# Kernel tuning notes

Hardware: AMD Instinct MI355X
Metric: run time of the kernel (lower is better)

Reference implementation:

```python
import jax, jax.numpy as jnp
import numpy as np

VOCAB, EMB, H, TRK, L, BOUND = 50257, 1024, 1024, 1024, 256, 25

def setup_inputs() -> dict:
    key = jax.random.key(0)
    ks = jax.random.split(key, 16)
    s = 0.02
    return {
        "query_words": jax.random.normal(ks[0], (L, 1, H), jnp.float32),
        "query_vector": jax.random.normal(ks[1], (1, 1, TRK), jnp.float32),
        "decision_vector": jax.random.normal(ks[2], (1, 1, H), jnp.float32),
        "target_answer": jax.random.randint(ks[3], (BOUND, 1, 1), 0, VOCAB, jnp.int64),
        "emb_table": jax.random.normal(ks[4], (VOCAB, EMB), jnp.float32) * s,
        "gru_Wih": jax.random.normal(ks[5], (3 * H, EMB + TRK), jnp.float32) * s,
        "gru_Whh": jax.random.normal(ks[6], (3 * H, H), jnp.float32) * s,
        "gru_bih": jnp.zeros((3 * H,), jnp.float32),
        "gru_bhh": jnp.zeros((3 * H,), jnp.float32),
        "attn_Wq": jax.random.normal(ks[7], (H, H), jnp.float32) * s,
        "attn_bq": jnp.zeros((H,), jnp.float32),
        "attn_Wk": jax.random.normal(ks[8], (H, H), jnp.float32) * s,
        "attn_bk": jnp.zeros((H,), jnp.float32),
        "attn_v": jax.random.normal(ks[9], (H,), jnp.float32) * s,
        "concat_W": jax.random.normal(ks[10], (H, 2 * H), jnp.float32) * s,
        "concat_b": jnp.zeros((H,), jnp.float32),
        "out_W": jax.random.normal(ks[11], (VOCAB, H), jnp.float32) * s,
        "out_b": jnp.zeros((VOCAB,), jnp.float32),
    }


def reference(query_words, query_vector, decision_vector, target_answer,
              emb_table, gru_Wih, gru_Whh, gru_bih, gru_bhh,
              attn_Wq, attn_bq, attn_Wk, attn_bk, attn_v,
              concat_W, concat_b, out_W, out_b):
    # eval-mode: dropout = identity; tf_ratio=1 -> teacher forcing for all steps
    h_dim = decision_vector.shape[-1]
    qw = query_words[:, 0, :]                      # [L, H] encoder memory
    keys = qw @ attn_Wk.T + attn_bk                # precompute key projection once
    qv = query_vector.reshape(-1)                  # [TRK]
    h0 = decision_vector.reshape(-1)               # [H]
    ta = target_answer.reshape(-1).astype(jnp.int32)
    # input token per step: SOS (0), then teacher-forced targets
    idx_seq = jnp.concatenate([jnp.zeros((1,), jnp.int32), ta[: BOUND - 1]])

    def step(h, idx):
        x = jnp.concatenate([qv, emb_table[idx]])  # cat(query_vector, embedded)
        g = gru_Wih @ x + gru_bih                  # [3H]
        gh = gru_Whh @ h + gru_bhh                 # [3H]
        r = jax.nn.sigmoid(g[:h_dim] + gh[:h_dim])
        z = jax.nn.sigmoid(g[h_dim:2 * h_dim] + gh[h_dim:2 * h_dim])
        n = jnp.tanh(g[2 * h_dim:] + r * gh[2 * h_dim:])
        h_new = (1.0 - z) * n + z * h
        # additive (Bahdanau) attention over query_words
        e = jnp.tanh(keys + attn_Wq @ h_new + attn_bq) @ attn_v  # [L]
        w = jax.nn.softmax(e)
        ctx = w @ qw                                              # [H]
        vec = jnp.tanh(concat_W @ jnp.concatenate([h_new, ctx]) + concat_b)
        logits = out_W @ vec + out_b                              # [VOCAB]
        return h_new, jax.nn.log_softmax(logits)

    _, logps = jax.lax.scan(step, h0, idx_seq)     # [BOUND, VOCAB]
    answer = jnp.argmax(logps, axis=-1)            # greedy tokens per step
    return (answer, logps)
```

## Files before the change

kernel.cpp:

```cpp
#include <hip/hip_runtime.h>
#include <math.h>

#define VOCAB 50257
#define EMB 1024
#define HD 1024
#define TRK 1024
#define LQ 256
#define BND 25

__device__ __forceinline__ float wred(float s){
  #pragma unroll
  for (int m = 32; m >= 1; m >>= 1) s += __shfl_xor(s, m, 64);
  return s;
}

__global__ __launch_bounds__(256) void k_pre(const float* __restrict__ Wih,
                                             const float* __restrict__ qv,
                                             const float* __restrict__ bih,
                                             const int*   __restrict__ ta,
                                             const float* __restrict__ emb,
                                             float* __restrict__ gib,
                                             float* __restrict__ E){
  int b = blockIdx.x, tid = threadIdx.x;
  if (b < 768){
    int w = tid >> 6, lane = tid & 63;
    int row = b*4 + w;
    const float* a = Wih + (size_t)row*2048;
    float s = 0.f;
    #pragma unroll
    for (int e = 0; e < 4; e++){
      int k = e*256 + lane*4;
      float4 av = *(const float4*)(a + k);
      float4 qr = *(const float4*)(qv + k);
      s += av.x*qr.x + av.y*qr.y + av.z*qr.z + av.w*qr.w;
    }
    s = wred(s);
    if (lane == 0) gib[row] = s + bih[row];
  } else {
    int g = (b - 768)*256 + tid;
    int t = g >> 10, i = g & 1023;
    int idx = (t == 0) ? 0 : ta[t-1];
    E[g] = emb[(size_t)idx*EMB + i];
  }
}

__global__ __launch_bounds__(256) void k_keys(const float* __restrict__ qw,
                                              const float* __restrict__ Wk,
                                              float* __restrict__ part){
  __shared__ float qt[64*256];
  int jb = blockIdx.x;
  int ks = blockIdx.y;
  int tid = threadIdx.x;
  int l = tid;
  float acc[16];
  #pragma unroll
  for (int j = 0; j < 16; j++) acc[j] = 0.f;

  for (int kt = 0; kt < 4; kt++){
    int kb = ks*256 + kt*64;
    __syncthreads();
    #pragma unroll
    for (int p = 0; p < 16; p++){
      int fidx = (p*256 + tid)*4;
      int kk = fidx & 63, ll = fidx >> 6;
      float4 v = *(const float4*)(qw + (size_t)ll*1024 + kb + kk);
      qt[(kk+0)*256 + (ll ^ ((kk+0)&31))] = v.x;
      qt[(kk+1)*256 + (ll ^ ((kk+1)&31))] = v.y;
      qt[(kk+2)*256 + (ll ^ ((kk+2)&31))] = v.z;
      qt[(kk+3)*256 + (ll ^ ((kk+3)&31))] = v.w;
    }
    __syncthreads();
    #pragma unroll
    for (int s = 0; s < 4; s++){
      float qr[16];
      #pragma unroll
      for (int q = 0; q < 16; q++){
        int k = s*16 + q;
        qr[q] = qt[k*256 + (l ^ (k&31))];
      }
      #pragma unroll
      for (int j = 0; j < 16; j++){
        const float* wr = Wk + (size_t)(jb*16 + j)*1024 + kb + s*16;
        #pragma unroll
        for (int q4 = 0; q4 < 4; q4++){
          float4 wv = *(const float4*)(wr + q4*4);
          acc[j] += qr[q4*4+0]*wv.x + qr[q4*4+1]*wv.y
                  + qr[q4*4+2]*wv.z + qr[q4*4+3]*wv.w;
        }
      }
    }
  }
  #pragma unroll
  for (int j = 0; j < 16; j++)
    part[((size_t)ks*1024 + jb*16 + j)*256 + l] = acc[j];
}

__global__ __launch_bounds__(256) void k_keys_red(const float* __restrict__ part,
                                                  const float* __restrict__ bk,
                                                  float* __restrict__ keysT){
  int g = blockIdx.x*256 + threadIdx.x;
  int base = g*4;
  float4 s0 = *(const float4*)(part + base);
  float4 s1 = *(const float4*)(part + 262144 + base);
  float4 s2 = *(const float4*)(part + 524288 + base);
  float4 s3 = *(const float4*)(part + 786432 + base);
  float b = bk[base >> 8];
  float4 r;
  r.x = s0.x + s1.x + s2.x + s3.x + b;
  r.y = s0.y + s1.y + s2.y + s3.y + b;
  r.z = s0.z + s1.z + s2.z + s3.z + b;
  r.w = s0.w + s1.w + s2.w + s3.w + b;
  *(float4*)(keysT + base) = r;
}

template<int K, int NCH>
__global__ __launch_bounds__(256) void k_gemm_s2(const float* __restrict__ A, int lda,
                                                 const float* __restrict__ B, int ldb,
                                                 const float* __restrict__ bias,
                                                 float* __restrict__ C,
                                                 int R, int N, int act){
  __shared__ float Bl[NCH*K];
  constexpr int KD4 = K/4;
  int tid = threadIdx.x, w = tid >> 6, lane = tid & 63;
  int row = blockIdx.x*4 + w;
  const float* a = A + (size_t)row*lda;
  float4 ar[K/256];
  #pragma unroll
  for (int e = 0; e < K/256; e++)
    ar[e] = *(const float4*)(a + e*256 + lane*4);
  float bs = bias[row];
  for (int c0 = 0; c0 < N; c0 += NCH){
    int nt = min(NCH, N - c0);
    __syncthreads();
    int total = nt*KD4;
    for (int i = tid; i < total; i += 256){
      int j = i/KD4, kk = i - j*KD4;
      *(float4*)&Bl[j*K + kk*4] = *(const float4*)(B + (size_t)(c0+j)*ldb + kk*4);
    }
    __syncthreads();
    for (int j = 0; j < nt; j++){
      float s = 0.f;
      #pragma unroll
      for (int e = 0; e < K/256; e++){
        float4 bv = *(const float4*)&Bl[j*K + e*256 + lane*4];
        s += ar[e].x*bv.x + ar[e].y*bv.y + ar[e].z*bv.z + ar[e].w*bv.w;
      }
      s = wred(s);
      if (lane == 0){
        float v = s + bs;
        if (act) v = tanhf(v);
        C[(size_t)(c0+j)*R + row] = v;
      }
    }
  }
}

__global__ __launch_bounds__(256, 2) void k_gru4(const float* __restrict__ Whh,
                                                 const float* __restrict__ bhh,
                                                 const float* __restrict__ gi,
                                                 const float* __restrict__ dv,
                                                 float* __restrict__ HC,
                                                 float* __restrict__ hx){
  __shared__ float Wl[12][1024];
  __shared__ float hbuf[1024];
  __shared__ float sres[12];
  int tid = threadIdx.x, w = tid >> 6, lane = tid & 63;
  int b = blockIdx.x;
  for (int i = tid; i < 3072; i += 256){
    int r = i >> 8, c = (i & 255)*4;
    int g = r >> 2, s = r & 3;
    *(float4*)&Wl[r][c] = *(const float4*)(Whh + (size_t)(g*1024 + b*4 + s)*1024 + c);
  }
  *(float4*)&hbuf[tid*4] = *(const float4*)(dv + tid*4);
  __syncthreads();

  for (int t = 0; t < BND; t++){
    float g0=0,g1=0,g2=0,bb0=0,bb1=0,bb2=0,hpown=0;
    if (tid < 4){
      int i = b*4 + tid;
      const float* gg = gi + (size_t)t*3072;
      g0 = gg[i]; g1 = gg[1024+i]; g2 = gg[2048+i];
      bb0 = bhh[i]; bb1 = bhh[1024+i]; bb2 = bhh[2048+i];
      hpown = hbuf[i];
    }
    float hv[16];
    #pragma unroll
    for (int e = 0; e < 4; e++){
      float4 v = *(const float4*)&hbuf[e*256 + lane*4];
      hv[e*4]=v.x; hv[e*4+1]=v.y; hv[e*4+2]=v.z; hv[e*4+3]=v.w;
    }
    #pragma unroll
    for (int j = 0; j < 3; j++){
      int r = w*3 + j;
      float a = 0.f;
      #pragma unroll
      for (int e = 0; e < 4; e++){
        float4 v = *(const float4*)&Wl[r][e*256 + lane*4];
        a += v.x*hv[e*4] + v.y*hv[e*4+1] + v.z*hv[e*4+2] + v.w*hv[e*4+3];
      }
      a = wred(a);
      if (lane == 0) sres[r] = a;
    }
    __syncthreads();
    if (tid < 4){
      int i = b*4 + tid;
      float ghr = sres[tid]   + bb0;
      float ghz = sres[4+tid] + bb1;
      float ghn = sres[8+tid] + bb2;
      float rr = 1.f/(1.f + expf(-(g0 + ghr)));
      float zz = 1.f/(1.f + expf(-(g1 + ghz)));
      float nn = tanhf(g2 + rr*ghn);
      float hnew = (1.f - zz)*nn + zz*hpown;
      HC[(size_t)t*2048 + i] = hnew;
      if (t < BND-1){
        __hip_atomic_store(hx + b*8 + tid, hnew, __ATOMIC_RELAXED, __HIP_MEMORY_SCOPE_AGENT);
        asm volatile("s_waitcnt vmcnt(0)" ::: "memory");
      }
    }
    if (t == BND-1) break;
    __syncthreads();
    if (tid == 0)
      __hip_atomic_store((int*)(hx + b*8 + 4), t+1, __ATOMIC_RELAXED, __HIP_MEMORY_SCOPE_AGENT);
    if (w == 0){
      for (;;){
        int f0 = __hip_atomic_load((const int*)(hx + (lane      )*8 + 4), __ATOMIC_RELAXED, __HIP_MEMORY_SCOPE_AGENT);
        int f1 = __hip_atomic_load((const int*)(hx + (64  + lane)*8 + 4), __ATOMIC_RELAXED, __HIP_MEMORY_SCOPE_AGENT);
        int f2 = __hip_atomic_load((const int*)(hx + (128 + lane)*8 + 4), __ATOMIC_RELAXED, __HIP_MEMORY_SCOPE_AGENT);
        int f3 = __hip_atomic_load((const int*)(hx + (192 + lane)*8 + 4), __ATOMIC_RELAXED, __HIP_MEMORY_SCOPE_AGENT);
        if (min(min(f0,f1),min(f2,f3)) >= t+1) break;
        __builtin_amdgcn_s_sleep(1);
      }
      #pragma unroll
      for (int q = 0; q < 4; q++){
        float d0 = __hip_atomic_load(hx + (q*64 + lane)*8 + 0, __ATOMIC_RELAXED, __HIP_MEMORY_SCOPE_AGENT);
        float d1 = __hip_atomic_load(hx + (q*64 + lane)*8 + 1, __ATOMIC_RELAXED, __HIP_MEMORY_SCOPE_AGENT);
        float d2 = __hip_atomic_load(hx + (q*64 + lane)*8 + 2, __ATOMIC_RELAXED, __HIP_MEMORY_SCOPE_AGENT);
        float d3 = __hip_atomic_load(hx + (q*64 + lane)*8 + 3, __ATOMIC_RELAXED, __HIP_MEMORY_SCOPE_AGENT);
        hbuf[q*256 + lane*4 + 0] = d0;
        hbuf[q*256 + lane*4 + 1] = d1;
        hbuf[q*256 + lane*4 + 2] = d2;
        hbuf[q*256 + lane*4 + 3] = d3;
      }
    }
    __syncthreads();
  }
}

__global__ __launch_bounds__(256) void k_attn1(const float* __restrict__ keysT,
                                               const float* __restrict__ Qt,
                                               const float* __restrict__ av,
                                               float* __restrict__ epart){
  int t = blockIdx.x, jc = blockIdx.y;
  int l = threadIdx.x;
  const float* q = Qt + (size_t)t*1024;
  int j0 = jc*32;
  float acc = 0.f;
  #pragma unroll
  for (int u = 0; u < 8; u++){
    int j = j0 + u*4;
    float k0 = keysT[(size_t)(j+0)*256 + l];
    float k1 = keysT[(size_t)(j+1)*256 + l];
    float k2 = keysT[(size_t)(j+2)*256 + l];
    float k3 = keysT[(size_t)(j+3)*256 + l];
    acc += tanhf(k0 + q[j+0]) * av[j+0]
         + tanhf(k1 + q[j+1]) * av[j+1]
         + tanhf(k2 + q[j+2]) * av[j+2]
         + tanhf(k3 + q[j+3]) * av[j+3];
  }
  epart[((size_t)t*32 + jc)*256 + l] = acc;
}

__global__ __launch_bounds__(256) void k_attn2(const float* __restrict__ epart,
                                               const float* __restrict__ qw,
                                               float* __restrict__ HC){
  __shared__ float red[256];
  __shared__ float sw[256];
  int t = blockIdx.x, tid = threadIdx.x;
  float e = 0.f;
  for (int jc = 0; jc < 32; jc++) e += epart[((size_t)t*32 + jc)*256 + tid];
  red[tid] = e; __syncthreads();
  for (int s = 128; s > 0; s >>= 1){
    if (tid < s) red[tid] = fmaxf(red[tid], red[tid+s]);
    __syncthreads();
  }
  float m = red[0]; __syncthreads();
  float wv = expf(e - m);
  red[tid] = wv; __syncthreads();
  for (int s = 128; s > 0; s >>= 1){
    if (tid < s) red[tid] += red[tid+s];
    __syncthreads();
  }
  float inv = 1.f/red[0];
  sw[tid] = wv*inv; __syncthreads();
  float4 c = make_float4(0.f,0.f,0.f,0.f);
  const float* qp = qw + tid*4;
  for (int ll = 0; ll < 256; ll++){
    float wl = sw[ll];
    float4 v = *(const float4*)(qp + (size_t)ll*1024);
    c.x += wl*v.x; c.y += wl*v.y; c.z += wl*v.z; c.w += wl*v.w;
  }
  *(float4*)(HC + (size_t)t*2048 + 1024 + tid*4) = c;
}

__global__ __launch_bounds__(256, 1) void k_gemm_big9(const float* __restrict__ A,
                                                      const float* __restrict__ B,
                                                      const float* __restrict__ bias,
                                                      float* __restrict__ C){
  __shared__ float Bl[25600];
  int tid = threadIdx.x;
  int rl = tid & 63;
  int q  = tid >> 6;
  int R0 = blockIdx.x*256;

  for (int i = tid; i < 6400; i += 256){
    int t = i >> 8, kk = (i & 255) << 2;
    *(float4*)&Bl[t*1024 + kk] = *(const float4*)(B + (size_t)t*1024 + kk);
  }

  const float* ap[4];
  #pragma unroll
  for (int j = 0; j < 4; j++){
    int r = R0 + 64*j + rl;
    if (r >= VOCAB) r = VOCAB-1;
    ap[j] = A + (size_t)r*1024 + q*256;
  }

  float acc[4][25];
  #pragma unroll
  for (int j = 0; j < 4; j++)
    #pragma unroll
    for (int t = 0; t < 25; t++) acc[j][t] = 0.f;

  float4 a[4][4];
  #pragma unroll
  for (int j = 0; j < 4; j++){
    a[j][0] = *(const float4*)(ap[j] + 0);
    a[j][1] = *(const float4*)(ap[j] + 4);
    a[j][2] = *(const float4*)(ap[j] + 8);
    a[j][3] = *(const float4*)(ap[j] + 12);
  }
  __syncthreads();

  const float* bq = Bl + q*256;
  #pragma unroll 1
  for (int kb = 0; kb < 256; kb += 16){
    float4 n[4][4];
    if (kb + 16 < 256){
      #pragma unroll
      for (int j = 0; j < 4; j++){
        n[j][0] = *(const float4*)(ap[j] + kb + 16);
        n[j][1] = *(const float4*)(ap[j] + kb + 20);
        n[j][2] = *(const float4*)(ap[j] + kb + 24);
        n[j][3] = *(const float4*)(ap[j] + kb + 28);
      }
    }
    #pragma unroll
    for (int t = 0; t < 25; t++){
      const float* bt = bq + t*1024 + kb;
      float4 b0 = *(const float4*)(bt + 0);
      float4 b1 = *(const float4*)(bt + 4);
      float4 b2 = *(const float4*)(bt + 8);
      float4 b3 = *(const float4*)(bt + 12);
      #pragma unroll
      for (int j = 0; j < 4; j++){
        acc[j][t] += a[j][0].x*b0.x + a[j][0].y*b0.y + a[j][0].z*b0.z + a[j][0].w*b0.w
                   + a[j][1].x*b1.x + a[j][1].y*b1.y + a[j][1].z*b1.z + a[j][1].w*b1.w
                   + a[j][2].x*b2.x + a[j][2].y*b2.y + a[j][2].z*b2.z + a[j][2].w*b2.w
                   + a[j][3].x*b3.x + a[j][3].y*b3.y + a[j][3].z*b3.z + a[j][3].w*b3.w;
      }
    }
    #pragma unroll
    for (int j = 0; j < 4; j++){
      a[j][0] = n[j][0]; a[j][1] = n[j][1]; a[j][2] = n[j][2]; a[j][3] = n[j][3];
    }
  }

  for (int tc0 = 0; tc0 < 25; tc0 += 13){
    int nt = min(13, 25 - tc0);
    __syncthreads();
    #pragma unroll
    for (int j = 0; j < 4; j++)
      for (int tt = 0; tt < nt; tt++)
        Bl[(q*256 + j*64 + rl)*13 + tt] = acc[j][tc0 + tt];
    __syncthreads();
    for (int v = tid; v < 256*nt; v += 256){
      int rr = v & 255, tt = v >> 8;
      float s = 0.f;
      #pragma unroll
      for (int qq = 0; qq < 4; qq++)
        s += Bl[(qq*256 + rr)*13 + tt];
      int row = R0 + rr;
      if (row < VOCAB)
        C[(size_t)(tc0 + tt)*VOCAB + row] = s + bias[row];
    }
  }
}

__global__ __launch_bounds__(256) void k_lstat(const float* __restrict__ C,
                                               float* __restrict__ pm,
                                               float* __restrict__ ps,
                                               int*   __restrict__ pa){
  __shared__ float sm[256], ss[256];
  __shared__ int   sa[256];
  int t = blockIdx.x, c = blockIdx.y, tid = threadIdx.x;
  int r0 = c*6283, r1 = min(r0 + 6283, VOCAB);
  const float* p = C + (size_t)t*VOCAB;
  float m = -3.4e38f, s = 0.f; int arg = r0;
  for (int r = r0 + tid; r < r1; r += 256){
    float x = p[r];
    if (x > m){ s = s*expf(m - x) + 1.f; m = x; arg = r; }
    else       s += expf(x - m);
  }
  sm[tid] = m; ss[tid] = s; sa[tid] = arg; __syncthreads();
  for (int st = 128; st > 0; st >>= 1){
    if (tid < st){
      float m1 = sm[tid], s1 = ss[tid]; int a1 = sa[tid];
      float m2 = sm[tid+st], s2 = ss[tid+st]; int a2 = sa[tid+st];
      if (m2 > m1){ sm[tid] = m2; ss[tid] = s2 + s1*expf(m1 - m2); sa[tid] = a2; }
      else if (m2 == m1){ ss[tid] = s1 + s2; sa[tid] = min(a1, a2); }
      else { ss[tid] = s1 + s2*expf(m2 - m1); }
    }
    __syncthreads();
  }
  if (tid == 0){ pm[t*8 + c] = sm[0]; ps[t*8 + c] = ss[0]; pa[t*8 + c] = sa[0]; }
}

__global__ void k_lfin(const float* __restrict__ pm, const float* __restrict__ ps,
                       const int* __restrict__ pa, float* __restrict__ Lg,
                       float* __restrict__ out){
  int t = threadIdx.x;
  if (t < 25){
    float M = pm[t*8], S = ps[t*8]; int A = pa[t*8];
    for (int c = 1; c < 8; c++){
      float m2 = pm[t*8+c], s2 = ps[t*8+c]; int a2 = pa[t*8+c];
      if (m2 > M){ S = s2 + S*expf(M - m2); M = m2; A = a2; }
      else if (m2 == M){ S += s2; A = min(A, a2); }
      else S += s2*expf(m2 - M);
    }
    Lg[t] = logf(S) + M;
    out[t] = (float)A;
  }
}

__global__ __launch_bounds__(256) void k_lsub(float* __restrict__ C,
                                              const float* __restrict__ Lg){
  int t = blockIdx.y;
  int r = blockIdx.x*256 + threadIdx.x;
  if (r < VOCAB) C[(size_t)t*VOCAB + r] -= Lg[t];
}

extern "C" void kernel_launch(void* const* d_in, const int* in_sizes, int n_in,
                              void* d_out, int out_size, void* d_ws, size_t ws_size,
                              hipStream_t stream){
  const float* qw  = (const float*)d_in[0];
  const float* qv  = (const float*)d_in[1];
  const float* dv  = (const float*)d_in[2];
  const int*   ta  = (const int*)d_in[3];
  const float* emb = (const float*)d_in[4];
  const float* Wih = (const float*)d_in[5];
  const float* Whh = (const float*)d_in[6];
  const float* bih = (const float*)d_in[7];
  const float* bhh = (const float*)d_in[8];
  const float* Wq  = (const float*)d_in[9];
  const float* bq  = (const float*)d_in[10];
  const float* Wk  = (const float*)d_in[11];
  const float* bk  = (const float*)d_in[12];
  const float* av  = (const float*)d_in[13];
  const float* cW  = (const float*)d_in[14];
  const float* cb  = (const float*)d_in[15];
  const float* oW  = (const float*)d_in[16];
  const float* ob  = (const float*)d_in[17];
  float* out = (float*)d_out;
  float* ws  = (float*)d_ws;

  float* part  = ws;
  float* ep    = ws;
  float* pm    = ws;
  float* ps    = ws + 256;
  int*   pa    = (int*)(ws + 512);
  float* Lg    = ws + 768;
  float* keysT = ws + 1048576;
  float* E     = ws + 1310720;
  float* gib   = ws + 1336320;
  float* gi    = ws + 1339392;
  float* HC    = ws + 1416192;
  float* Qt    = ws + 1467392;
  float* VEC   = ws + 1492992;
  float* hx    = ws + 1518592;

  hipMemsetAsync(hx, 0, 2048*4, stream);
  k_pre<<<868, 256, 0, stream>>>(Wih, qv, bih, ta, emb, gib, E);
  k_keys<<<dim3(64,4), 256, 0, stream>>>(qw, Wk, part);
  k_keys_red<<<256, 256, 0, stream>>>(part, bk, keysT);
  k_gemm_s2<1024,16><<<768, 256, 0, stream>>>(Wih + 1024, 2048, E, 1024, gib, gi, 3072, 25, 0);
  k_gru4<<<256, 256, 0, stream>>>(Whh, bhh, gi, dv, HC, hx);
  k_gemm_s2<1024,16><<<256, 256, 0, stream>>>(Wq, 1024, HC, 2048, bq, Qt, 1024, 25, 0);
  k_attn1<<<dim3(25,32), 256, 0, stream>>>(keysT, Qt, av, ep);
  k_attn2<<<25, 256, 0, stream>>>(ep, qw, HC);
  k_gemm_s2<2048,8><<<256, 256, 0, stream>>>(cW, 2048, HC, 2048, cb, VEC, 1024, 25, 1);
  k_gemm_big9<<<197, 256, 0, stream>>>(oW, VEC, ob, out + 25);
  k_lstat<<<dim3(25,8), 256, 0, stream>>>(out + 25, pm, ps, pa);
  k_lfin<<<1, 64, 0, stream>>>(pm, ps, pa, Lg, out);
  k_lsub<<<dim3(197,25), 256, 0, stream>>>(out + 25, Lg);
}
```

Measured before the change: 424.1 us.

## Split output-projection GEMM along K into two halves for more blocks

The vocab projection GEMM is split along the reduction dimension: each row tile gets two blocks, each covering half of K, with smaller shared memory. The two partial results are written to a workspace buffer and to the output, then summed with the bias inside the log-softmax stat and subtract kernels. This doubles the block count from 197 to 394 so more of the GPU's compute units are busy. The cost is extra traffic for the second partial logits array, read in both the stat and subtract passes.

```diff
diff --git a/kernel.cpp b/kernel.cpp
--- a/kernel.cpp
+++ b/kernel.cpp
@@ -302,19 +302,21 @@
   *(float4*)(HC + (size_t)t*2048 + 1024 + tid*4) = c;
 }
 
-__global__ __launch_bounds__(256, 1) void k_gemm_big9(const float* __restrict__ A,
-                                                      const float* __restrict__ B,
-                                                      const float* __restrict__ bias,
-                                                      float* __restrict__ C){
-  __shared__ float Bl[25600];
+__global__ __launch_bounds__(256, 1) void k_gemm_big10(const float* __restrict__ A,
+                                                       const float* __restrict__ B,
+                                                       float* __restrict__ P0,
+                                                       float* __restrict__ P1){
+  __shared__ float Bl[13312];
   int tid = threadIdx.x;
   int rl = tid & 63;
   int q  = tid >> 6;
-  int R0 = blockIdx.x*256;
-
-  for (int i = tid; i < 6400; i += 256){
-    int t = i >> 8, kk = (i & 255) << 2;
-    *(float4*)&Bl[t*1024 + kk] = *(const float4*)(B + (size_t)t*1024 + kk);
+  int half = blockIdx.x & 1;
+  int R0 = (blockIdx.x >> 1)*256;
+  float* P = half ? P1 : P0;
+
+  for (int i = tid; i < 3200; i += 256){
+    int t = i >> 7, kk = (i & 127) << 2;
+    *(float4*)&Bl[t*512 + kk] = *(const float4*)(B + (size_t)t*1024 + half*512 + kk);
   }
 
   const float* ap[4];
@@ -322,7 +324,7 @@
   for (int j = 0; j < 4; j++){
     int r = R0 + 64*j + rl;
     if (r >= VOCAB) r = VOCAB-1;
-    ap[j] = A + (size_t)r*1024 + q*256;
+    ap[j] = A + (size_t)r*1024 + half*512 + q*128;
   }
 
   float acc[4][25];
@@ -341,11 +343,11 @@
   }
   __syncthreads();
 
-  const float* bq = Bl + q*256;
+  const float* bq = Bl + q*128;
   #pragma unroll 1
-  for (int kb = 0; kb < 256; kb += 16){
+  for (int kb = 0; kb < 128; kb += 16){
     float4 n[4][4];
-    if (kb + 16 < 256){
+    if (kb + 16 < 128){
       #pragma unroll
       for (int j = 0; j < 4; j++){
         n[j][0] = *(const float4*)(ap[j] + kb + 16);
@@ -356,7 +358,7 @@
     }
     #pragma unroll
     for (int t = 0; t < 25; t++){
-      const float* bt = bq + t*1024 + kb;
+      const float* bt = bq + t*512 + kb;
       float4 b0 = *(const float4*)(bt + 0);
       float4 b1 = *(const float4*)(bt + 4);
       float4 b2 = *(const float4*)(bt + 8);
@@ -391,12 +393,14 @@
         s += Bl[(qq*256 + rr)*13 + tt];
       int row = R0 + rr;
       if (row < VOCAB)
-        C[(size_t)(tc0 + tt)*VOCAB + row] = s + bias[row];
-    }
-  }
-}
-
-__global__ __launch_bounds__(256) void k_lstat(const float* __restrict__ C,
+        P[(size_t)(tc0 + tt)*VOCAB + row] = s;
+    }
+  }
+}
+
+__global__ __launch_bounds__(256) void k_lstat(const float* __restrict__ P0,
+                                               const float* __restrict__ P1,
+                                               const float* __restrict__ ob,
                                                float* __restrict__ pm,
                                                float* __restrict__ ps,
                                                int*   __restrict__ pa){
@@ -404,10 +408,11 @@
   __shared__ int   sa[256];
   int t = blockIdx.x, c = blockIdx.y, tid = threadIdx.x;
   int r0 = c*6283, r1 = min(r0 + 6283, VOCAB);
-  const float* p = C + (size_t)t*VOCAB;
+  const float* p0 = P0 + (size_t)t*VOCAB;
+  const float* p1 = P1 + (size_t)t*VOCAB;
   float m = -3.4e38f, s = 0.f; int arg = r0;
   for (int r = r0 + tid; r < r1; r += 256){
-    float x = p[r];
+    float x = p0[r] + p1[r] + ob[r];
     if (x > m){ s = s*expf(m - x) + 1.f; m = x; arg = r; }
     else       s += expf(x - m);
   }
@@ -442,11 +447,16 @@
   }
 }
 
-__global__ __launch_bounds__(256) void k_lsub(float* __restrict__ C,
+__global__ __launch_bounds__(256) void k_lsub(const float* __restrict__ P0,
+                                              float* __restrict__ C,
+                                              const float* __restrict__ ob,
                                               const float* __restrict__ Lg){
   int t = blockIdx.y;
   int r = blockIdx.x*256 + threadIdx.x;
-  if (r < VOCAB) C[(size_t)t*VOCAB + r] -= Lg[t];
+  if (r < VOCAB){
+    size_t idx = (size_t)t*VOCAB + r;
+    C[idx] = P0[idx] + C[idx] + ob[r] - Lg[t];
+  }
 }
 
 extern "C" void kernel_launch(void* const* d_in, const int* in_sizes, int n_in,
@@ -475,10 +485,7 @@
 
   float* part  = ws;
   float* ep    = ws;
-  float* pm    = ws;
-  float* ps    = ws + 256;
-  int*   pa    = (int*)(ws + 512);
-  float* Lg    = ws + 768;
+  float* P0    = ws;
   float* keysT = ws + 1048576;
   float* E     = ws + 1310720;
   float* gib   = ws + 1336320;
@@ -487,6 +494,10 @@
   float* Qt    = ws + 1467392;
   float* VEC   = ws + 1492992;
   float* hx    = ws + 1518592;
+  float* pm    = ws + 1520640;
+  float* ps    = ws + 1520896;
+  int*   pa    = (int*)(ws + 1521152);
+  float* Lg    = ws + 1521408;
 
   hipMemsetAsync(hx, 0, 2048*4, stream);
   k_pre<<<868, 256, 0, stream>>>(Wih, qv, bih, ta, emb, gib, E);
@@ -498,8 +509,8 @@
   k_attn1<<<dim3(25,32), 256, 0, stream>>>(keysT, Qt, av, ep);
   k_attn2<<<25, 256, 0, stream>>>(ep, qw, HC);
   k_gemm_s2<2048,8><<<256, 256, 0, stream>>>(cW, 2048, HC, 2048, cb, VEC, 1024, 25, 1);
-  k_gemm_big9<<<197, 256, 0, stream>>>(oW, VEC, ob, out + 25);
-  k_lstat<<<dim3(25,8), 256, 0, stream>>>(out + 25, pm, ps, pa);
+  k_gemm_big10<<<394, 256, 0, stream>>>(oW, VEC, P0, out + 25);
+  k_lstat<<<dim3(25,8), 256, 0, stream>>>(P0, out + 25, ob, pm, ps, pa);
   k_lfin<<<1, 64, 0, stream>>>(pm, ps, pa, Lg, out);
-  k_lsub<<<dim3(197,25), 256, 0, stream>>>(out + 25, Lg);
-}
+  k_lsub<<<dim3(197,25), 256, 0, stream>>>(P0, out + 25, ob, Lg);
+}
```

After: 445.5 us. 1.05x slower.

## Use sentinel-valued per-step hidden buffers for GRU sync; split output GEMM K across 8 waves

Applied to the files above, without the earlier changes.

The GRU recurrence no longer uses per-block step flags with a barrier and a flag-polling loop. Each step writes hidden values into a fresh per-timestep slot pre-filled with a sentinel pattern, and readers spin until the data words themselves are not the sentinel, which removes a barrier and a round of flag traffic per step. The large vocabulary GEMM now runs 512-thread blocks, with each wave covering 128 K elements instead of 256, doubling in-block parallelism and shortening each thread's K loop. In exchange the final reduction across waves is larger, the memset now clears a much bigger buffer, and a float whose bit pattern equals the sentinel is nudged by one bit.

```diff
diff --git a/kernel.cpp b/kernel.cpp
--- a/kernel.cpp
+++ b/kernel.cpp
@@ -7,6 +7,7 @@
 #define TRK 1024
 #define LQ 256
 #define BND 25
+#define SENT 0xAAAAAAAAu
 
 __device__ __forceinline__ float wred(float s){
   #pragma unroll
@@ -155,12 +156,12 @@
   }
 }
 
-__global__ __launch_bounds__(256, 2) void k_gru4(const float* __restrict__ Whh,
+__global__ __launch_bounds__(256, 2) void k_gru5(const float* __restrict__ Whh,
                                                  const float* __restrict__ bhh,
                                                  const float* __restrict__ gi,
                                                  const float* __restrict__ dv,
                                                  float* __restrict__ HC,
-                                                 float* __restrict__ hx){
+                                                 unsigned* __restrict__ hxu){
   __shared__ float Wl[12][1024];
   __shared__ float hbuf[1024];
   __shared__ float sres[12];
@@ -213,33 +214,31 @@
       float hnew = (1.f - zz)*nn + zz*hpown;
       HC[(size_t)t*2048 + i] = hnew;
       if (t < BND-1){
-        __hip_atomic_store(hx + b*8 + tid, hnew, __ATOMIC_RELAXED, __HIP_MEMORY_SCOPE_AGENT);
+        union { float f; unsigned u; } cv; cv.f = hnew;
+        if (cv.u == SENT) cv.u ^= 1u;
+        __hip_atomic_store(hxu + (size_t)t*2048 + b*8 + tid, cv.u,
+                           __ATOMIC_RELAXED, __HIP_MEMORY_SCOPE_AGENT);
         asm volatile("s_waitcnt vmcnt(0)" ::: "memory");
       }
     }
     if (t == BND-1) break;
-    __syncthreads();
-    if (tid == 0)
-      __hip_atomic_store((int*)(hx + b*8 + 4), t+1, __ATOMIC_RELAXED, __HIP_MEMORY_SCOPE_AGENT);
     if (w == 0){
-      for (;;){
-        int f0 = __hip_atomic_load((const int*)(hx + (lane      )*8 + 4), __ATOMIC_RELAXED, __HIP_MEMORY_SCOPE_AGENT);
-        int f1 = __hip_atomic_load((const int*)(hx + (64  + lane)*8 + 4), __ATOMIC_RELAXED, __HIP_MEMORY_SCOPE_AGENT);
-        int f2 = __hip_atomic_load((const int*)(hx + (128 + lane)*8 + 4), __ATOMIC_RELAXED, __HIP_MEMORY_SCOPE_AGENT);
-        int f3 = __hip_atomic_load((const int*)(hx + (192 + lane)*8 + 4), __ATOMIC_RELAXED, __HIP_MEMORY_SCOPE_AGENT);
-        if (min(min(f0,f1),min(f2,f3)) >= t+1) break;
-        __builtin_amdgcn_s_sleep(1);
-      }
+      const unsigned* base = hxu + (size_t)t*2048;
       #pragma unroll
       for (int q = 0; q < 4; q++){
-        float d0 = __hip_atomic_load(hx + (q*64 + lane)*8 + 0, __ATOMIC_RELAXED, __HIP_MEMORY_SCOPE_AGENT);
-        float d1 = __hip_atomic_load(hx + (q*64 + lane)*8 + 1, __ATOMIC_RELAXED, __HIP_MEMORY_SCOPE_AGENT);
-        float d2 = __hip_atomic_load(hx + (q*64 + lane)*8 + 2, __ATOMIC_RELAXED, __HIP_MEMORY_SCOPE_AGENT);
-        float d3 = __hip_atomic_load(hx + (q*64 + lane)*8 + 3, __ATOMIC_RELAXED, __HIP_MEMORY_SCOPE_AGENT);
-        hbuf[q*256 + lane*4 + 0] = d0;
-        hbuf[q*256 + lane*4 + 1] = d1;
-        hbuf[q*256 + lane*4 + 2] = d2;
-        hbuf[q*256 + lane*4 + 3] = d3;
+        int line = q*64 + lane;
+        unsigned d0, d1, d2, d3;
+        for (;;){
+          d0 = __hip_atomic_load(base + line*8 + 0, __ATOMIC_RELAXED, __HIP_MEMORY_SCOPE_AGENT);
+          d1 = __hip_atomic_load(base + line*8 + 1, __ATOMIC_RELAXED, __HIP_MEMORY_SCOPE_AGENT);
+          d2 = __hip_atomic_load(base + line*8 + 2, __ATOMIC_RELAXED, __HIP_MEMORY_SCOPE_AGENT);
+          d3 = __hip_atomic_load(base + line*8 + 3, __ATOMIC_RELAXED, __HIP_MEMORY_SCOPE_AGENT);
+          if (d0 != SENT && d1 != SENT && d2 != SENT && d3 != SENT) break;
+        }
+        hbuf[line*4 + 0] = __uint_as_float(d0);
+        hbuf[line*4 + 1] = __uint_as_float(d1);
+        hbuf[line*4 + 2] = __uint_as_float(d2);
+        hbuf[line*4 + 3] = __uint_as_float(d3);
       }
     }
     __syncthreads();
@@ -302,17 +301,17 @@
   *(float4*)(HC + (size_t)t*2048 + 1024 + tid*4) = c;
 }
 
-__global__ __launch_bounds__(256, 1) void k_gemm_big9(const float* __restrict__ A,
-                                                      const float* __restrict__ B,
-                                                      const float* __restrict__ bias,
-                                                      float* __restrict__ C){
-  __shared__ float Bl[25600];
+__global__ __launch_bounds__(512, 1) void k_gemm_big12(const float* __restrict__ A,
+                                                       const float* __restrict__ B,
+                                                       const float* __restrict__ bias,
+                                                       float* __restrict__ C){
+  __shared__ float Bl[26624];
   int tid = threadIdx.x;
   int rl = tid & 63;
-  int q  = tid >> 6;
+  int w  = tid >> 6;
   int R0 = blockIdx.x*256;
 
-  for (int i = tid; i < 6400; i += 256){
+  for (int i = tid; i < 6400; i += 512){
     int t = i >> 8, kk = (i & 255) << 2;
     *(float4*)&Bl[t*1024 + kk] = *(const float4*)(B + (size_t)t*1024 + kk);
   }
@@ -322,7 +321,7 @@
   for (int j = 0; j < 4; j++){
     int r = R0 + 64*j + rl;
     if (r >= VOCAB) r = VOCAB-1;
-    ap[j] = A + (size_t)r*1024 + q*256;
+    ap[j] = A + (size_t)r*1024 + w*128;
   }
 
   float acc[4][25];
@@ -341,11 +340,11 @@
   }
   __syncthreads();
 
-  const float* bq = Bl + q*256;
+  const float* bw = Bl + w*128;
   #pragma unroll 1
-  for (int kb = 0; kb < 256; kb += 16){
+  for (int kb = 0; kb < 128; kb += 16){
     float4 n[4][4];
-    if (kb + 16 < 256){
+    if (kb + 16 < 128){
       #pragma unroll
       for (int j = 0; j < 4; j++){
         n[j][0] = *(const float4*)(ap[j] + kb + 16);
@@ -356,7 +355,7 @@
     }
     #pragma unroll
     for (int t = 0; t < 25; t++){
-      const float* bt = bq + t*1024 + kb;
+      const float* bt = bw + t*1024 + kb;
       float4 b0 = *(const float4*)(bt + 0);
       float4 b1 = *(const float4*)(bt + 4);
       float4 b2 = *(const float4*)(bt + 8);
@@ -381,14 +380,14 @@
     #pragma unroll
     for (int j = 0; j < 4; j++)
       for (int tt = 0; tt < nt; tt++)
-        Bl[(q*256 + j*64 + rl)*13 + tt] = acc[j][tc0 + tt];
-    __syncthreads();
-    for (int v = tid; v < 256*nt; v += 256){
+        Bl[(w*256 + j*64 + rl)*13 + tt] = acc[j][tc0 + tt];
+    __syncthreads();
+    for (int v = tid; v < 256*nt; v += 512){
       int rr = v & 255, tt = v >> 8;
       float s = 0.f;
       #pragma unroll
-      for (int qq = 0; qq < 4; qq++)
-        s += Bl[(qq*256 + rr)*13 + tt];
+      for (int ww = 0; ww < 8; ww++)
+        s += Bl[(ww*256 + rr)*13 + tt];
       int row = R0 + rr;
       if (row < VOCAB)
         C[(size_t)(tc0 + tt)*VOCAB + row] = s + bias[row];
@@ -475,10 +474,6 @@
 
   float* part  = ws;
   float* ep    = ws;
-  float* pm    = ws;
-  float* ps    = ws + 256;
-  int*   pa    = (int*)(ws + 512);
-  float* Lg    = ws + 768;
   float* keysT = ws + 1048576;
   float* E     = ws + 1310720;
   float* gib   = ws + 1336320;
@@ -486,19 +481,23 @@
   float* HC    = ws + 1416192;
   float* Qt    = ws + 1467392;
   float* VEC   = ws + 1492992;
-  float* hx    = ws + 1518592;
-
-  hipMemsetAsync(hx, 0, 2048*4, stream);
+  unsigned* hx = (unsigned*)(ws + 1518592);
+  float* pm    = ws + 1569792;
+  float* ps    = ws + 1570048;
+  int*   pa    = (int*)(ws + 1570304);
+  float* Lg    = ws + 1570560;
+
+  hipMemsetAsync(hx, 0xAA, 51200*4, stream);
   k_pre<<<868, 256, 0, stream>>>(Wih, qv, bih, ta, emb, gib, E);
   k_keys<<<dim3(64,4), 256, 0, stream>>>(qw, Wk, part);
   k_keys_red<<<256, 256, 0, stream>>>(part, bk, keysT);
   k_gemm_s2<1024,16><<<768, 256, 0, stream>>>(Wih + 1024, 2048, E, 1024, gib, gi, 3072, 25, 0);
-  k_gru4<<<256, 256, 0, stream>>>(Whh, bhh, gi, dv, HC, hx);
+  k_gru5<<<256, 256, 0, stream>>>(Whh, bhh, gi, dv, HC, hx);
   k_gemm_s2<1024,16><<<256, 256, 0, stream>>>(Wq, 1024, HC, 2048, bq, Qt, 1024, 25, 0);
   k_attn1<<<dim3(25,32), 256, 0, stream>>>(keysT, Qt, av, ep);
   k_attn2<<<25, 256, 0, stream>>>(ep, qw, HC);
   k_gemm_s2<2048,8><<<256, 256, 0, stream>>>(cW, 2048, HC, 2048, cb, VEC, 1024, 25, 1);
-  k_gemm_big9<<<197, 256, 0, stream>>>(oW, VEC, ob, out + 25);
+  k_gemm_big12<<<197, 512, 0, stream>>>(oW, VEC, ob, out + 25);
   k_lstat<<<dim3(25,8), 256, 0, stream>>>(out + 25, pm, ps, pa);
   k_lfin<<<1, 64, 0, stream>>>(pm, ps, pa, Lg, out);
   k_lsub<<<dim3(197,25), 256, 0, stream>>>(out + 25, Lg);
```

Measured after the change: 424.4 us. No clear change (+0.1%).

## Fuse prelude kernels, use sentinel-based GRU sync with 128 larger blocks

Applied to the files above, without the earlier changes.

Merges the Wih·qv, embedding gather and key-projection kernels into one launch. The keys reduction is folded into the attention score kernel, and the log-sum finalize is folded into the subtraction kernel. The persistent GRU kernel now runs 128 blocks of 512 threads with 8 rows each. It replaces the per-step flag-then-data handshake with per-step buffers that are pre-filled with a sentinel pattern, and consumers spin until the data itself is non-sentinel. This removes launches and one round of cross-block latency per recurrent step. The costs are a larger memset, redundant partial-sum reads in attention, and reliance on the sentinel never being a real value, which is guarded by flipping a bit.

```diff
diff --git a/kernel.cpp b/kernel.cpp
--- a/kernel.cpp
+++ b/kernel.cpp
@@ -7,6 +7,7 @@
 #define TRK 1024
 #define LQ 256
 #define BND 25
+#define SENT 0xAAAAAAAAu
 
 __device__ __forceinline__ float wred(float s){
   #pragma unroll
@@ -14,13 +15,17 @@
   return s;
 }
 
-__global__ __launch_bounds__(256) void k_pre(const float* __restrict__ Wih,
-                                             const float* __restrict__ qv,
-                                             const float* __restrict__ bih,
-                                             const int*   __restrict__ ta,
-                                             const float* __restrict__ emb,
-                                             float* __restrict__ gib,
-                                             float* __restrict__ E){
+__global__ __launch_bounds__(256) void k_pre_keys(const float* __restrict__ Wih,
+                                                  const float* __restrict__ qv,
+                                                  const float* __restrict__ bih,
+                                                  const int*   __restrict__ ta,
+                                                  const float* __restrict__ emb,
+                                                  const float* __restrict__ qw,
+                                                  const float* __restrict__ Wk,
+                                                  float* __restrict__ gib,
+                                                  float* __restrict__ E,
+                                                  float* __restrict__ part){
+  __shared__ float qt[64*256];
   int b = blockIdx.x, tid = threadIdx.x;
   if (b < 768){
     int w = tid >> 6, lane = tid & 63;
@@ -36,21 +41,18 @@
     }
     s = wred(s);
     if (lane == 0) gib[row] = s + bih[row];
-  } else {
+    return;
+  }
+  if (b < 868){
     int g = (b - 768)*256 + tid;
     int t = g >> 10, i = g & 1023;
     int idx = (t == 0) ? 0 : ta[t-1];
     E[g] = emb[(size_t)idx*EMB + i];
-  }
-}
-
-__global__ __launch_bounds__(256) void k_keys(const float* __restrict__ qw,
-                                              const float* __restrict__ Wk,
-                                              float* __restrict__ part){
-  __shared__ float qt[64*256];
-  int jb = blockIdx.x;
-  int ks = blockIdx.y;
-  int tid = threadIdx.x;
+    return;
+  }
+  int b2 = b - 868;
+  int jb = b2 & 63;
+  int ks = b2 >> 6;
   int l = tid;
   float acc[16];
   #pragma unroll
@@ -93,24 +95,6 @@
   #pragma unroll
   for (int j = 0; j < 16; j++)
     part[((size_t)ks*1024 + jb*16 + j)*256 + l] = acc[j];
-}
-
-__global__ __launch_bounds__(256) void k_keys_red(const float* __restrict__ part,
-                                                  const float* __restrict__ bk,
-                                                  float* __restrict__ keysT){
-  int g = blockIdx.x*256 + threadIdx.x;
-  int base = g*4;
-  float4 s0 = *(const float4*)(part + base);
-  float4 s1 = *(const float4*)(part + 262144 + base);
-  float4 s2 = *(const float4*)(part + 524288 + base);
-  float4 s3 = *(const float4*)(part + 786432 + base);
-  float b = bk[base >> 8];
-  float4 r;
-  r.x = s0.x + s1.x + s2.x + s3.x + b;
-  r.y = s0.y + s1.y + s2.y + s3.y + b;
-  r.z = s0.z + s1.z + s2.z + s3.z + b;
-  r.w = s0.w + s1.w + s2.w + s3.w + b;
-  *(float4*)(keysT + base) = r;
 }
 
 template<int K, int NCH>
@@ -155,29 +139,30 @@
   }
 }
 
-__global__ __launch_bounds__(256, 2) void k_gru4(const float* __restrict__ Whh,
+__global__ __launch_bounds__(512, 1) void k_gru6(const float* __restrict__ Whh,
                                                  const float* __restrict__ bhh,
                                                  const float* __restrict__ gi,
                                                  const float* __restrict__ dv,
                                                  float* __restrict__ HC,
-                                                 float* __restrict__ hx){
-  __shared__ float Wl[12][1024];
+                                                 unsigned* __restrict__ hxu){
+  __shared__ float Wl[24][1024];
   __shared__ float hbuf[1024];
-  __shared__ float sres[12];
+  __shared__ float sres[24];
   int tid = threadIdx.x, w = tid >> 6, lane = tid & 63;
   int b = blockIdx.x;
-  for (int i = tid; i < 3072; i += 256){
+  for (int i = tid; i < 6144; i += 512){
     int r = i >> 8, c = (i & 255)*4;
-    int g = r >> 2, s = r & 3;
-    *(float4*)&Wl[r][c] = *(const float4*)(Whh + (size_t)(g*1024 + b*4 + s)*1024 + c);
-  }
-  *(float4*)&hbuf[tid*4] = *(const float4*)(dv + tid*4);
+    int g = r >> 3, s = r & 7;
+    *(float4*)&Wl[r][c] = *(const float4*)(Whh + (size_t)(g*1024 + b*8 + s)*1024 + c);
+  }
+  if (tid < 256)
+    *(float4*)&hbuf[tid*4] = *(const float4*)(dv + tid*4);
   __syncthreads();
 
   for (int t = 0; t < BND; t++){
     float g0=0,g1=0,g2=0,bb0=0,bb1=0,bb2=0,hpown=0;
-    if (tid < 4){
-      int i = b*4 + tid;
+    if (tid < 8){
+      int i = b*8 + tid;
       const float* gg = gi + (size_t)t*3072;
       g0 = gg[i]; g1 = gg[1024+i]; g2 = gg[2048+i];
       bb0 = bhh[i]; bb1 = bhh[1024+i]; bb2 = bhh[2048+i];
@@ -202,51 +187,52 @@
       if (lane == 0) sres[r] = a;
     }
     __syncthreads();
-    if (tid < 4){
-      int i = b*4 + tid;
-      float ghr = sres[tid]   + bb0;
-      float ghz = sres[4+tid] + bb1;
-      float ghn = sres[8+tid] + bb2;
+    if (tid < 8){
+      int i = b*8 + tid;
+      float ghr = sres[tid]      + bb0;
+      float ghz = sres[8  + tid] + bb1;
+      float ghn = sres[16 + tid] + bb2;
       float rr = 1.f/(1.f + expf(-(g0 + ghr)));
       float zz = 1.f/(1.f + expf(-(g1 + ghz)));
       float nn = tanhf(g2 + rr*ghn);
       float hnew = (1.f - zz)*nn + zz*hpown;
       HC[(size_t)t*2048 + i] = hnew;
       if (t < BND-1){
-        __hip_atomic_store(hx + b*8 + tid, hnew, __ATOMIC_RELAXED, __HIP_MEMORY_SCOPE_AGENT);
+        union { float f; unsigned u; } cv; cv.f = hnew;
+        if (cv.u == SENT) cv.u ^= 1u;
+        __hip_atomic_store(hxu + (size_t)t*2048 + b*16 + tid, cv.u,
+                           __ATOMIC_RELAXED, __HIP_MEMORY_SCOPE_AGENT);
         asm volatile("s_waitcnt vmcnt(0)" ::: "memory");
       }
     }
     if (t == BND-1) break;
-    __syncthreads();
-    if (tid == 0)
-      __hip_atomic_store((int*)(hx + b*8 + 4), t+1, __ATOMIC_RELAXED, __HIP_MEMORY_SCOPE_AGENT);
     if (w == 0){
-      for (;;){
-        int f0 = __hip_atomic_load((const int*)(hx + (lane      )*8 + 4), __ATOMIC_RELAXED, __HIP_MEMORY_SCOPE_AGENT);
-        int f1 = __hip_atomic_load((const int*)(hx + (64  + lane)*8 + 4), __ATOMIC_RELAXED, __HIP_MEMORY_SCOPE_AGENT);
-        int f2 = __hip_atomic_load((const int*)(hx + (128 + lane)*8 + 4), __ATOMIC_RELAXED, __HIP_MEMORY_SCOPE_AGENT);
-        int f3 = __hip_atomic_load((const int*)(hx + (192 + lane)*8 + 4), __ATOMIC_RELAXED, __HIP_MEMORY_SCOPE_AGENT);
-        if (min(min(f0,f1),min(f2,f3)) >= t+1) break;
-        __builtin_amdgcn_s_sleep(1);
-      }
-      #pragma unroll
-      for (int q = 0; q < 4; q++){
-        float d0 = __hip_atomic_load(hx + (q*64 + lane)*8 + 0, __ATOMIC_RELAXED, __HIP_MEMORY_SCOPE_AGENT);
-        float d1 = __hip_atomic_load(hx + (q*64 + lane)*8 + 1, __ATOMIC_RELAXED, __HIP_MEMORY_SCOPE_AGENT);
-        float d2 = __hip_atomic_load(hx + (q*64 + lane)*8 + 2, __ATOMIC_RELAXED, __HIP_MEMORY_SCOPE_AGENT);
-        float d3 = __hip_atomic_load(hx + (q*64 + lane)*8 + 3, __ATOMIC_RELAXED, __HIP_MEMORY_SCOPE_AGENT);
-        hbuf[q*256 + lane*4 + 0] = d0;
-        hbuf[q*256 + lane*4 + 1] = d1;
-        hbuf[q*256 + lane*4 + 2] = d2;
-        hbuf[q*256 + lane*4 + 3] = d3;
-      }
-    }
-    __syncthreads();
-  }
-}
-
-__global__ __launch_bounds__(256) void k_attn1(const float* __restrict__ keysT,
+      const unsigned* base = hxu + (size_t)t*2048;
+      #pragma unroll
+      for (int q = 0; q < 2; q++){
+        int blk = q*64 + lane;
+        const unsigned* bp = base + blk*16;
+        unsigned d[8];
+        for (;;){
+          bool ok = true;
+          #pragma unroll
+          for (int j = 0; j < 8; j++){
+            d[j] = __hip_atomic_load(bp + j, __ATOMIC_RELAXED, __HIP_MEMORY_SCOPE_AGENT);
+            ok = ok && (d[j] != SENT);
+          }
+          if (ok) break;
+        }
+        #pragma unroll
+        for (int j = 0; j < 8; j++)
+          hbuf[blk*8 + j] = __uint_as_float(d[j]);
+      }
+    }
+    __syncthreads();
+  }
+}
+
+__global__ __launch_bounds__(256) void k_attn1(const float* __restrict__ part,
+                                               const float* __restrict__ bk,
                                                const float* __restrict__ Qt,
                                                const float* __restrict__ av,
                                                float* __restrict__ epart){
@@ -257,15 +243,16 @@
   float acc = 0.f;
   #pragma unroll
   for (int u = 0; u < 8; u++){
-    int j = j0 + u*4;
-    float k0 = keysT[(size_t)(j+0)*256 + l];
-    float k1 = keysT[(size_t)(j+1)*256 + l];
-    float k2 = keysT[(size_t)(j+2)*256 + l];
-    float k3 = keysT[(size_t)(j+3)*256 + l];
-    acc += tanhf(k0 + q[j+0]) * av[j+0]
-         + tanhf(k1 + q[j+1]) * av[j+1]
-         + tanhf(k2 + q[j+2]) * av[j+2]
-         + tanhf(k3 + q[j+3]) * av[j+3];
+    #pragma unroll
+    for (int v = 0; v < 4; v++){
+      int j = j0 + u*4 + v;
+      float kv = part[(size_t)j*256 + l]
+               + part[(size_t)(1024+j)*256 + l]
+               + part[(size_t)(2048+j)*256 + l]
+               + part[(size_t)(3072+j)*256 + l]
+               + bk[j];
+      acc += tanhf(kv + q[j]) * av[j];
+    }
   }
   epart[((size_t)t*32 + jc)*256 + l] = acc;
 }
@@ -425,28 +412,24 @@
   if (tid == 0){ pm[t*8 + c] = sm[0]; ps[t*8 + c] = ss[0]; pa[t*8 + c] = sa[0]; }
 }
 
-__global__ void k_lfin(const float* __restrict__ pm, const float* __restrict__ ps,
-                       const int* __restrict__ pa, float* __restrict__ Lg,
-                       float* __restrict__ out){
-  int t = threadIdx.x;
-  if (t < 25){
-    float M = pm[t*8], S = ps[t*8]; int A = pa[t*8];
-    for (int c = 1; c < 8; c++){
-      float m2 = pm[t*8+c], s2 = ps[t*8+c]; int a2 = pa[t*8+c];
-      if (m2 > M){ S = s2 + S*expf(M - m2); M = m2; A = a2; }
-      else if (m2 == M){ S += s2; A = min(A, a2); }
-      else S += s2*expf(m2 - M);
-    }
-    Lg[t] = logf(S) + M;
-    out[t] = (float)A;
-  }
-}
-
-__global__ __launch_bounds__(256) void k_lsub(float* __restrict__ C,
-                                              const float* __restrict__ Lg){
+__global__ __launch_bounds__(256) void k_lsub2(float* __restrict__ C,
+                                               const float* __restrict__ pm,
+                                               const float* __restrict__ ps,
+                                               const int* __restrict__ pa,
+                                               float* __restrict__ out){
   int t = blockIdx.y;
+  float M = pm[t*8], S = ps[t*8]; int A = pa[t*8];
+  #pragma unroll
+  for (int c = 1; c < 8; c++){
+    float m2 = pm[t*8+c], s2 = ps[t*8+c]; int a2 = pa[t*8+c];
+    if (m2 > M){ S = s2 + S*expf(M - m2); M = m2; A = a2; }
+    else if (m2 == M){ S += s2; A = min(A, a2); }
+    else S += s2*expf(m2 - M);
+  }
+  float Lg = logf(S) + M;
   int r = blockIdx.x*256 + threadIdx.x;
-  if (r < VOCAB) C[(size_t)t*VOCAB + r] -= Lg[t];
+  if (r < VOCAB) C[(size_t)t*VOCAB + r] -= Lg;
+  if (blockIdx.x == 0 && threadIdx.x == 0) out[t] = (float)A;
 }
 
 extern "C" void kernel_launch(void* const* d_in, const int* in_sizes, int n_in,
@@ -474,32 +457,27 @@
   float* ws  = (float*)d_ws;
 
   float* part  = ws;
-  float* ep    = ws;
-  float* pm    = ws;
-  float* ps    = ws + 256;
-  int*   pa    = (int*)(ws + 512);
-  float* Lg    = ws + 768;
-  float* keysT = ws + 1048576;
+  float* ep    = ws + 1048576;
   float* E     = ws + 1310720;
   float* gib   = ws + 1336320;
   float* gi    = ws + 1339392;
   float* HC    = ws + 1416192;
   float* Qt    = ws + 1467392;
   float* VEC   = ws + 1492992;
-  float* hx    = ws + 1518592;
-
-  hipMemsetAsync(hx, 0, 2048*4, stream);
-  k_pre<<<868, 256, 0, stream>>>(Wih, qv, bih, ta, emb, gib, E);
-  k_keys<<<dim3(64,4), 256, 0, stream>>>(qw, Wk, part);
-  k_keys_red<<<256, 256, 0, stream>>>(part, bk, keysT);
+  unsigned* hx = (unsigned*)(ws + 1518592);
+  float* pm    = ws + 1569792;
+  float* ps    = ws + 1570048;
+  int*   pa    = (int*)(ws + 1570304);
+
+  hipMemsetAsync(hx, 0xAA, 51200*4, stream);
+  k_pre_keys<<<1124, 256, 0, stream>>>(Wih, qv, bih, ta, emb, qw, Wk, gib, E, part);
   k_gemm_s2<1024,16><<<768, 256, 0, stream>>>(Wih + 1024, 2048, E, 1024, gib, gi, 3072, 25, 0);
-  k_gru4<<<256, 256, 0, stream>>>(Whh, bhh, gi, dv, HC, hx);
+  k_gru6<<<128, 512, 0, stream>>>(Whh, bhh, gi, dv, HC, hx);
   k_gemm_s2<1024,16><<<256, 256, 0, stream>>>(Wq, 1024, HC, 2048, bq, Qt, 1024, 25, 0);
-  k_attn1<<<dim3(25,32), 256, 0, stream>>>(keysT, Qt, av, ep);
+  k_attn1<<<dim3(25,32), 256, 0, stream>>>(part, bk, Qt, av, ep);
   k_attn2<<<25, 256, 0, stream>>>(ep, qw, HC);
   k_gemm_s2<2048,8><<<256, 256, 0, stream>>>(cW, 2048, HC, 2048, cb, VEC, 1024, 25, 1);
   k_gemm_big9<<<197, 256, 0, stream>>>(oW, VEC, ob, out + 25);
   k_lstat<<<dim3(25,8), 256, 0, stream>>>(out + 25, pm, ps, pa);
-  k_lfin<<<1, 64, 0, stream>>>(pm, ps, pa, Lg, out);
-  k_lsub<<<dim3(197,25), 256, 0, stream>>>(out + 25, Lg);
-}
+  k_lsub2<<<dim3(197,25), 256, 0, stream>>>(out + 25, pm, ps, pa, out);
+}
```

After: 415.1 us. -2.1%, faster.
